# Optimization experiments

Measured on AMD Instinct MI355X. Metric: run time of the kernel, lower is better.

## Reference

```python
import jax, jax.numpy as jnp
import numpy as np

N = 100000
E = 500000
HID = 256
N_EDGE_TYPES = 5
N_ATOM = 16
N_CHARGE = 7
NUM_RBF = 16
CUTOFF = 5.0
LN_EPS = 1e-5


def _xavier(key, shape):
    fan_in, fan_out = shape[0], shape[1]
    lim = float(np.sqrt(6.0 / (fan_in + fan_out)))
    return jax.random.uniform(key, shape, jnp.float32, -lim, lim)


def setup_inputs() -> dict:
    key = jax.random.key(0)
    ks = jax.random.split(key, 12)
    input_dim = HID * 2 + NUM_RBF + N_ATOM + N_CHARGE  # 551
    h = jax.random.normal(ks[0], (N, HID), jnp.float32)
    x = jax.random.normal(ks[1], (N, 3), jnp.float32)
    spawn_node_idx = jax.random.randint(ks[2], (E,), 0, N)
    existing_node_idx = jax.random.randint(ks[3], (E,), 0, N)
    ins_x = jax.random.normal(ks[4], (E, 3), jnp.float32)
    ins_a = jax.random.randint(ks[5], (E,), 0, N_ATOM)
    ins_c = jax.random.randint(ks[6], (E,), 0, N_CHARGE)
    # MLP params (Xavier weights, zero biases; LayerNorm gamma=1, beta=0)
    W1 = _xavier(ks[7], (input_dim, HID)); b1 = jnp.zeros((HID,), jnp.float32)
    g1 = jnp.ones((HID,), jnp.float32); be1 = jnp.zeros((HID,), jnp.float32)
    W2 = _xavier(ks[8], (HID, HID // 2)); b2 = jnp.zeros((HID // 2,), jnp.float32)
    g2 = jnp.ones((HID // 2,), jnp.float32); be2 = jnp.zeros((HID // 2,), jnp.float32)
    W3 = _xavier(ks[9], (HID // 2, N_EDGE_TYPES)); b3 = jnp.zeros((N_EDGE_TYPES,), jnp.float32)
    # Gaussian RBF parameters: centers on [0, cutoff], shared width from spacing
    rbf_mu = jnp.linspace(0.0, CUTOFF, NUM_RBF).astype(jnp.float32)
    delta = CUTOFF / (NUM_RBF - 1)
    rbf_gamma = jnp.asarray(1.0 / (2.0 * delta * delta), jnp.float32)
    return {"h": h, "x": x, "spawn_node_idx": spawn_node_idx,
            "existing_node_idx": existing_node_idx, "ins_x": ins_x,
            "ins_a": ins_a, "ins_c": ins_c,
            "W1": W1, "b1": b1, "g1": g1, "be1": be1,
            "W2": W2, "b2": b2, "g2": g2, "be2": be2,
            "W3": W3, "b3": b3, "rbf_mu": rbf_mu, "rbf_gamma": rbf_gamma}


def _layer_norm(z, gamma, beta):
    mu = jnp.mean(z, axis=-1, keepdims=True)
    var = jnp.mean((z - mu) ** 2, axis=-1, keepdims=True)
    return (z - mu) * jax.lax.rsqrt(var + LN_EPS) * gamma + beta


def reference(h, x, spawn_node_idx, existing_node_idx, ins_x, ins_a, ins_c,
              W1, b1, g1, be1, W2, b2, g2, be2, W3, b3, rbf_mu, rbf_gamma):
    # gather node pairs  [E, HID] / [E, 3]
    h_spawn = h[spawn_node_idx]
    h_existing = h[existing_node_idx]
    existing_pos = x[existing_node_idx]
    # distance + Gaussian RBF  [E, NUM_RBF]
    d = jnp.maximum(jnp.linalg.norm(ins_x - existing_pos, axis=-1), 1e-6)
    dist_features = jnp.exp(-rbf_gamma * (d[:, None] - rbf_mu) ** 2)
    # one-hot insertion type features
    ins_atom = jax.nn.one_hot(ins_a, N_ATOM, dtype=h.dtype)
    ins_charge = jax.nn.one_hot(ins_c, N_CHARGE, dtype=h.dtype)
    feats = jnp.concatenate([h_spawn, h_existing, dist_features, ins_atom, ins_charge], axis=-1)
    # 3-layer MLP: Linear -> LN -> SiLU -> Linear -> LN -> SiLU -> Linear
    z = jax.nn.silu(_layer_norm(feats @ W1 + b1, g1, be1))
    z = jax.nn.silu(_layer_norm(z @ W2 + b2, g2, be2))
    return z @ W3 + b3  # [E, N_EDGE_TYPES]
```

## Files before the change

### kernel.cpp

```cpp
#include <hip/hip_runtime.h>
#include <stdint.h>

#define NN 100000
#define EE 500000
#define HIDD 256
#define LN_EPS 1e-5f

typedef _Float16 half8 __attribute__((ext_vector_type(8)));
typedef _Float16 half4 __attribute__((ext_vector_type(4)));
typedef __fp16 fp16x2 __attribute__((ext_vector_type(2)));
typedef float f32x4 __attribute__((ext_vector_type(4)));
typedef float f32x2 __attribute__((ext_vector_type(2)));

#define LBAR() asm volatile("s_waitcnt lgkmcnt(0)\n\ts_barrier" ::: "memory")

__device__ __forceinline__ unsigned short f2h(float f) {
  _Float16 h = (_Float16)f;
  union { _Float16 hh; unsigned short us; } u; u.hh = h;
  return u.us;
}

__device__ __forceinline__ unsigned pkrtz(float a, float b) {
  union { fp16x2 h; unsigned u; } c;
  c.h = __builtin_amdgcn_cvt_pkrtz(a, b);
  return c.u;
}

__device__ __forceinline__ float fast_silu(float y) {
  float e = __expf(-y);
  return y * __builtin_amdgcn_rcpf(1.f + e);
}

__device__ __forceinline__ half8 ldg8(const unsigned short* p) {
  return *(const half8*)p;
}

__device__ __forceinline__ int4 cvt_row(const float* s) {
  float4 a0 = *(const float4*)s, a1 = *(const float4*)(s + 4);
  uint4 ua;
  ua.x = pkrtz(a0.x, a0.y); ua.y = pkrtz(a0.z, a0.w);
  ua.z = pkrtz(a1.x, a1.y); ua.w = pkrtz(a1.z, a1.w);
  return *(int4*)&ua;
}

__global__ __launch_bounds__(256) void prep_kern(const float* __restrict__ h,
                                                 const float* __restrict__ W1,
                                                 const float* __restrict__ W2,
                                                 const float* __restrict__ W3,
                                                 unsigned short* __restrict__ hb,
                                                 unsigned short* __restrict__ w1sw,
                                                 unsigned short* __restrict__ w2sw,
                                                 unsigned short* __restrict__ w3sw) {
  int b = blockIdx.x;
  if (b < 712) {
    int t = b * 256 + threadIdx.x;
    if (t < 147456) {
      int chunk = t >> 14, rem = t & 16383;
      int kq = rem >> 11, n = (rem >> 3) & 255, j = rem & 7;
      int k = (chunk << 6) + (kq << 3) + j;
      float v = (k < 551) ? W1[k * 256 + n] : 0.f;
      w1sw[t] = f2h(v);
    } else if (t < 147456 + 32768) {
      int t2 = t - 147456;
      int chunk = t2 >> 13, rem = t2 & 8191;
      int kq = rem >> 10, n = (rem >> 3) & 127, j = rem & 7;
      int k = (chunk << 6) + (kq << 3) + j;
      w2sw[t2] = f2h(W2[k * 128 + n]);
    } else if (t < 147456 + 32768 + 2048) {
      int t3 = t - 180224;
      int kq = t3 >> 7, o = (t3 >> 3) & 15, j = t3 & 7;
      int k = (kq << 3) + j;
      w3sw[t3] = f2h((o < 5) ? W3[k * 5 + o] : 0.f);
    }
  } else {
    int i = ((b - 712) * 256 + threadIdx.x) * 8;
    float4 v0 = *(const float4*)(h + i);
    float4 v1 = *(const float4*)(h + i + 4);
    uint4 u;
    u.x = pkrtz(v0.x, v0.y); u.y = pkrtz(v0.z, v0.w);
    u.z = pkrtz(v1.x, v1.y); u.w = pkrtz(v1.z, v1.w);
    *(uint4*)(hb + i) = u;
  }
}

struct __align__(16) SMem {
  short r1[16384];
  short feats[4096];
  float red[512];
  _Float16 b1h[256], g1h[256], be1h[256];
  _Float16 b2h[128], g2h[128], be2h[128];
  float muv[16];
  float b3v[8];
  int spI[64], exI[64];
};

__global__ __launch_bounds__(256, 3)
void edge_head_main(const float* __restrict__ h, const float* __restrict__ x,
                    const int* __restrict__ spawn, const int* __restrict__ exist,
                    const float* __restrict__ insx, const int* __restrict__ insa,
                    const int* __restrict__ insc,
                    const float* __restrict__ b1, const float* __restrict__ g1,
                    const float* __restrict__ be1,
                    const float* __restrict__ b2, const float* __restrict__ g2,
                    const float* __restrict__ be2,
                    const float* __restrict__ b3, const float* __restrict__ mu,
                    const float* __restrict__ gammaP,
                    const unsigned short* __restrict__ w1sw,
                    const unsigned short* __restrict__ w2sw,
                    const unsigned short* __restrict__ w3swg,
                    const unsigned short* __restrict__ hb, int use_hb,
                    float* __restrict__ out) {
  __shared__ SMem sm;
  const int t = threadIdx.x;
  const int base = blockIdx.x * 64;
  const int lane = t & 63;
  const int wv = t >> 6;
  const int cl = lane & 15;
  const int q = lane >> 4;
  const int sx = (cl & 7) << 3;

  sm.b1h[t] = (_Float16)b1[t]; sm.g1h[t] = (_Float16)g1[t]; sm.be1h[t] = (_Float16)be1[t];
  if (t < 128) { sm.b2h[t] = (_Float16)b2[t]; sm.g2h[t] = (_Float16)g2[t]; sm.be2h[t] = (_Float16)be2[t]; }
  if (t < 16) sm.muv[t] = mu[t];
  if (t < 8) sm.b3v[t] = (t < 5) ? b3[t] : 0.f;
  if (t < 64) {
    int e = base + t; int ec = e < EE ? e : EE - 1;
    sm.spI[t] = spawn[ec]; sm.exI[t] = exist[ec];
  }
  const float gma = gammaP[0];

  LBAR();

  float dreg = 0.f;
  int k1 = 16, k2 = 32;
  if (t < 64) {
    int e = base + t; int ec = e < EE ? e : EE - 1;
    float ix0 = insx[ec * 3], ix1 = insx[ec * 3 + 1], ix2 = insx[ec * 3 + 2];
    int nd = sm.exI[t];
    float dx = ix0 - x[nd * 3], dy = ix1 - x[nd * 3 + 1], dz = ix2 - x[nd * 3 + 2];
    dreg = fmaxf(sqrtf(dx * dx + dy * dy + dz * dz), 1e-6f);
    k1 = 16 + insa[ec]; k2 = 32 + insc[ec];
  }

  const int row0 = t >> 3, p0 = t & 7;
  const int row1 = row0 + 32;
  const int sw0 = ((p0 ^ (row0 & 7)) << 3);
  const int sw1 = ((p0 ^ (row1 & 7)) << 3);

  const size_t oSp0 = (size_t)sm.spI[row0] * HIDD + p0 * 8;
  const size_t oSp1 = (size_t)sm.spI[row1] * HIDD + p0 * 8;
  const size_t oEx0 = (size_t)sm.exI[row0] * HIDD + p0 * 8;
  const size_t oEx1 = (size_t)sm.exI[row1] * HIDD + p0 * 8;
  const char* bSp0 = use_hb ? (const char*)(hb + oSp0) : (const char*)(h + oSp0);
  const char* bSp1 = use_hb ? (const char*)(hb + oSp1) : (const char*)(h + oSp1);
  const char* bEx0 = use_hb ? (const char*)(hb + oEx0) : (const char*)(h + oEx0);
  const char* bEx1 = use_hb ? (const char*)(hb + oEx1) : (const char*)(h + oEx1);

  int4 pS0, pS1, pS2, pS3;
#define GLOAD2(ph) do {                                                 \
    const char* b0_ = ((ph) < 2) ? bSp0 : bEx0;                         \
    const char* b1_ = ((ph) < 2) ? bSp1 : bEx1;                         \
    const int ce_ = ((ph) & 1) * 128;             \
    if (use_hb) {                                                       \
      pS0 = *(const int4*)(b0_ + ce_ * 2);                              \
      pS1 = *(const int4*)(b1_ + ce_ * 2);                              \
      pS2 = *(const int4*)(b0_ + (ce_ + 64) * 2);                       \
      pS3 = *(const int4*)(b1_ + (ce_ + 64) * 2);                       \
    } else {                                                            \
      pS0 = cvt_row((const float*)(b0_ + ce_ * 4));                     \
      pS1 = cvt_row((const float*)(b1_ + ce_ * 4));                     \
      pS2 = cvt_row((const float*)(b0_ + (ce_ + 64) * 4));              \
      pS3 = cvt_row((const float*)(b1_ + (ce_ + 64) * 4));              \
    }                                                                   \
  } while (0)

  GLOAD2(0);
  *(int4*)&sm.r1[row0 * 64 + sw0] = pS0;
  *(int4*)&sm.r1[row1 * 64 + sw1] = pS1;
  *(int4*)&sm.r1[4096 + row0 * 64 + sw0] = pS2;
  *(int4*)&sm.r1[4096 + row1 * 64 + sw1] = pS3;
  GLOAD2(1);

  const unsigned short* w1p = w1sw + q * 2048 + wv * 512 + cl * 8;

  if (t < 64) {
    short* rp = &sm.feats[t * 64];
    const int sw = t & 7;
    float rb[16];
#pragma unroll
    for (int k = 0; k < 16; ++k) { float dd = dreg - sm.muv[k]; rb[k] = __expf(-gma * dd * dd); }
    uint4 ua, ub;
    ua.x = pkrtz(rb[0], rb[1]);  ua.y = pkrtz(rb[2], rb[3]);
    ua.z = pkrtz(rb[4], rb[5]);  ua.w = pkrtz(rb[6], rb[7]);
    ub.x = pkrtz(rb[8], rb[9]);  ub.y = pkrtz(rb[10], rb[11]);
    ub.z = pkrtz(rb[12], rb[13]); ub.w = pkrtz(rb[14], rb[15]);
    *(int4*)&rp[(0 ^ sw) * 8] = *(int4*)&ua;
    *(int4*)&rp[(1 ^ sw) * 8] = *(int4*)&ub;
    const int4 z4 = {0, 0, 0, 0};
#pragma unroll
    for (int g = 2; g < 8; ++g) *(int4*)&rp[(g ^ sw) * 8] = z4;
    rp[((k1 >> 3) ^ sw) * 8 + (k1 & 7)] = (short)0x3C00;
    rp[((k2 >> 3) ^ sw) * 8 + (k2 & 7)] = (short)0x3C00;
  }

  LBAR();

  f32x4 acc[4][4];
#pragma unroll
  for (int i = 0; i < 4; ++i)
#pragma unroll
    for (int j = 0; j < 4; ++j) acc[i][j] = (f32x4){0.f, 0.f, 0.f, 0.f};

#pragma unroll
  for (int p = 0; p < 4; ++p) {
    if (p < 3) {
      const int nb = ((p + 1) & 1) * 8192;
      *(int4*)&sm.r1[nb + row0 * 64 + sw0] = pS0;
      *(int4*)&sm.r1[nb + row1 * 64 + sw1] = pS1;
      *(int4*)&sm.r1[nb + 4096 + row0 * 64 + sw0] = pS2;
      *(int4*)&sm.r1[nb + 4096 + row1 * 64 + sw1] = pS3;
      if (p < 2) GLOAD2(p + 2);
    }
    const int cb = (p & 1) * 8192;
#pragma unroll
    for (int ch = 0; ch < 2; ++ch) {
      const unsigned short* wp = w1p + (2 * p + ch) * 16384;
#pragma unroll
      for (int ks = 0; ks < 2; ++ks) {
        half8 bf[4], fX[4];
#pragma unroll
        for (int j = 0; j < 4; ++j)
          bf[j] = *(const half8*)&sm.r1[cb + ch * 4096 + (j * 16 + cl) * 64 + ((ks * 32 + q * 8) ^ sx)];
#pragma unroll
        for (int i = 0; i < 4; ++i) fX[i] = ldg8(wp + ks * 8192 + i * 128);
#pragma unroll
        for (int i = 0; i < 4; ++i)
#pragma unroll
          for (int j = 0; j < 4; ++j)
            acc[i][j] = __builtin_amdgcn_mfma_f32_16x16x32_f16(fX[i], bf[j], acc[i][j], 0, 0, 0);
      }
    }
    if (p < 3) LBAR();
  }
#undef GLOAD2

  {
    const unsigned short* wp = w1p + 8 * 16384;
#pragma unroll
    for (int ks = 0; ks < 2; ++ks) {
      half8 bf[4], fX[4];
#pragma unroll
      for (int j = 0; j < 4; ++j)
        bf[j] = *(const half8*)&sm.feats[(j * 16 + cl) * 64 + ((ks * 32 + q * 8) ^ sx)];
#pragma unroll
      for (int i = 0; i < 4; ++i) fX[i] = ldg8(wp + ks * 8192 + i * 128);
#pragma unroll
      for (int i = 0; i < 4; ++i)
#pragma unroll
        for (int j = 0; j < 4; ++j)
          acc[i][j] = __builtin_amdgcn_mfma_f32_16x16x32_f16(fX[i], bf[j], acc[i][j], 0, 0, 0);
    }
  }

  f32x2 bb1[4][2];
#pragma unroll
  for (int i = 0; i < 4; ++i) {
    half4 b4 = *(const half4*)&sm.b1h[wv * 64 + i * 16 + q * 4];
    bb1[i][0] = (f32x2){(float)b4[0], (float)b4[1]};
    bb1[i][1] = (f32x2){(float)b4[2], (float)b4[3]};
  }
  float S1arr[4], Q1arr[4];
#pragma unroll
  for (int j = 0; j < 4; ++j) {
    f32x2 S2 = (f32x2){0.f, 0.f}, Q2 = (f32x2){0.f, 0.f};
#pragma unroll
    for (int i = 0; i < 4; ++i) {
      f32x2 v0 = (f32x2){acc[i][j][0], acc[i][j][1]} + bb1[i][0];
      f32x2 v1 = (f32x2){acc[i][j][2], acc[i][j][3]} + bb1[i][1];
      acc[i][j][0] = v0[0]; acc[i][j][1] = v0[1];
      acc[i][j][2] = v1[0]; acc[i][j][3] = v1[1];
      S2 += v0 + v1;
      Q2 += v0 * v0;
      Q2 += v1 * v1;
    }
    float S = S2[0] + S2[1], Q = Q2[0] + Q2[1];
    S += __shfl_xor(S, 16); S += __shfl_xor(S, 32);
    Q += __shfl_xor(Q, 16); Q += __shfl_xor(Q, 32);
    S1arr[j] = S; Q1arr[j] = Q;
  }
  if (q == 0) {
#pragma unroll
    for (int j = 0; j < 4; ++j) {
      sm.red[wv * 64 + j * 16 + cl] = S1arr[j];
      sm.red[256 + wv * 64 + j * 16 + cl] = Q1arr[j];
    }
  }
  LBAR();
  f32x2 rs1[4], mr1[4];
#pragma unroll
  for (int j = 0; j < 4; ++j) {
    int m = j * 16 + cl;
    float S = sm.red[m] + sm.red[64 + m] + sm.red[128 + m] + sm.red[192 + m];
    float Q = sm.red[256 + m] + sm.red[320 + m] + sm.red[384 + m] + sm.red[448 + m];
    float mn = S * (1.f / 256.f);
    float rs = rsqrtf(Q * (1.f / 256.f) - mn * mn + LN_EPS);
    rs1[j] = (f32x2){rs, rs};
    mr1[j] = (f32x2){-mn * rs, -mn * rs};
  }
#pragma unroll
  for (int i = 0; i < 4; ++i) {
    half4 g4 = *(const half4*)&sm.g1h[wv * 64 + i * 16 + q * 4];
    half4 e4 = *(const half4*)&sm.be1h[wv * 64 + i * 16 + q * 4];
    f32x2 gg0 = (f32x2){(float)g4[0], (float)g4[1]}, gg1 = (f32x2){(float)g4[2], (float)g4[3]};
    f32x2 ee0 = (f32x2){(float)e4[0], (float)e4[1]}, ee1 = (f32x2){(float)e4[2], (float)e4[3]};
#pragma unroll
    for (int j = 0; j < 4; ++j) {
      f32x2 v0 = (f32x2){acc[i][j][0], acc[i][j][1]};
      f32x2 v1 = (f32x2){acc[i][j][2], acc[i][j][3]};
      f32x2 t0 = v0 * rs1[j] + mr1[j];
      f32x2 t1 = v1 * rs1[j] + mr1[j];
      f32x2 y0 = t0 * gg0 + ee0;
      f32x2 y1 = t1 * gg1 + ee1;
      float s0 = fast_silu(y0[0]), s1 = fast_silu(y0[1]);
      float s2 = fast_silu(y1[0]), s3 = fast_silu(y1[1]);
      uint2 w; w.x = pkrtz(s0, s1); w.y = pkrtz(s2, s3);
      int m = j * 16 + cl;
      int k0 = wv * 64 + i * 16 + q * 4;
      *(uint2*)&sm.r1[m * 256 + (k0 ^ ((m & 7) << 3))] = w;
    }
  }
  LBAR();

  half8 af3[4];
#pragma unroll
  for (int ks = 0; ks < 4; ++ks)
    af3[ks] = ldg8(w3swg + (ks * 4 + q) * 128 + cl * 8);

  const unsigned short* w2p = w2sw + q * 1024 + wv * 256 + cl * 8;
  f32x4 acc2[2][4];
#pragma unroll
  for (int i = 0; i < 2; ++i)
#pragma unroll
    for (int j = 0; j < 4; ++j) acc2[i][j] = (f32x4){0.f, 0.f, 0.f, 0.f};
#pragma unroll
  for (int c2 = 0; c2 < 4; ++c2) {
#pragma unroll
    for (int ks = 0; ks < 2; ++ks) {
      half8 a0 = ldg8(w2p + c2 * 8192 + ks * 4096);
      half8 a1 = ldg8(w2p + c2 * 8192 + ks * 4096 + 128);
      half8 bf[4];
#pragma unroll
      for (int j = 0; j < 4; ++j)
        bf[j] = *(const half8*)&sm.r1[(j * 16 + cl) * 256 + ((c2 * 64 + ks * 32 + q * 8) ^ sx)];
#pragma unroll
      for (int j = 0; j < 4; ++j) {
        acc2[0][j] = __builtin_amdgcn_mfma_f32_16x16x32_f16(a0, bf[j], acc2[0][j], 0, 0, 0);
        acc2[1][j] = __builtin_amdgcn_mfma_f32_16x16x32_f16(a1, bf[j], acc2[1][j], 0, 0, 0);
      }
    }
  }

  f32x2 bb2[2][2];
#pragma unroll
  for (int i = 0; i < 2; ++i) {
    half4 b4 = *(const half4*)&sm.b2h[wv * 32 + i * 16 + q * 4];
    bb2[i][0] = (f32x2){(float)b4[0], (float)b4[1]};
    bb2[i][1] = (f32x2){(float)b4[2], (float)b4[3]};
  }
  float S2arr[4], Q2arr[4];
#pragma unroll
  for (int j = 0; j < 4; ++j) {
    f32x2 S2 = (f32x2){0.f, 0.f}, Q2 = (f32x2){0.f, 0.f};
#pragma unroll
    for (int i = 0; i < 2; ++i) {
      f32x2 v0 = (f32x2){acc2[i][j][0], acc2[i][j][1]} + bb2[i][0];
      f32x2 v1 = (f32x2){acc2[i][j][2], acc2[i][j][3]} + bb2[i][1];
      acc2[i][j][0] = v0[0]; acc2[i][j][1] = v0[1];
      acc2[i][j][2] = v1[0]; acc2[i][j][3] = v1[1];
      S2 += v0 + v1;
      Q2 += v0 * v0;
      Q2 += v1 * v1;
    }
    float S = S2[0] + S2[1], Q = Q2[0] + Q2[1];
    S += __shfl_xor(S, 16); S += __shfl_xor(S, 32);
    Q += __shfl_xor(Q, 16); Q += __shfl_xor(Q, 32);
    S2arr[j] = S; Q2arr[j] = Q;
  }
  if (q == 0) {
#pragma unroll
    for (int j = 0; j < 4; ++j) {
      sm.red[wv * 64 + j * 16 + cl] = S2arr[j];
      sm.red[256 + wv * 64 + j * 16 + cl] = Q2arr[j];
    }
  }
  LBAR();
  f32x2 rs2[4], mr2[4];
#pragma unroll
  for (int j = 0; j < 4; ++j) {
    int m = j * 16 + cl;
    float S = sm.red[m] + sm.red[64 + m] + sm.red[128 + m] + sm.red[192 + m];
    float Q = sm.red[256 + m] + sm.red[320 + m] + sm.red[384 + m] + sm.red[448 + m];
    float mn = S * (1.f / 128.f);
    float rs = rsqrtf(Q * (1.f / 128.f) - mn * mn + LN_EPS);
    rs2[j] = (f32x2){rs, rs};
    mr2[j] = (f32x2){-mn * rs, -mn * rs};
  }
#pragma unroll
  for (int i = 0; i < 2; ++i) {
    half4 g4 = *(const half4*)&sm.g2h[wv * 32 + i * 16 + q * 4];
    half4 e4 = *(const half4*)&sm.be2h[wv * 32 + i * 16 + q * 4];
    f32x2 gg0 = (f32x2){(float)g4[0], (float)g4[1]}, gg1 = (f32x2){(float)g4[2], (float)g4[3]};
    f32x2 ee0 = (f32x2){(float)e4[0], (float)e4[1]}, ee1 = (f32x2){(float)e4[2], (float)e4[3]};
#pragma unroll
    for (int j = 0; j < 4; ++j) {
      f32x2 v0 = (f32x2){acc2[i][j][0], acc2[i][j][1]};
      f32x2 v1 = (f32x2){acc2[i][j][2], acc2[i][j][3]};
      f32x2 t0 = v0 * rs2[j] + mr2[j];
      f32x2 t1 = v1 * rs2[j] + mr2[j];
      f32x2 y0 = t0 * gg0 + ee0;
      f32x2 y1 = t1 * gg1 + ee1;
      float s0 = fast_silu(y0[0]), s1 = fast_silu(y0[1]);
      float s2 = fast_silu(y1[0]), s3 = fast_silu(y1[1]);
      uint2 w; w.x = pkrtz(s0, s1); w.y = pkrtz(s2, s3);
      int m = j * 16 + cl;
      int k0 = wv * 32 + i * 16 + q * 4;
      *(uint2*)&sm.r1[m * 128 + (k0 ^ ((m & 7) << 3))] = w;
    }
  }
  LBAR();

  f32x4 a3 = (f32x4){0.f, 0.f, 0.f, 0.f};
  const int m3 = wv * 16 + cl;
  const int sx3 = (m3 & 7) << 3;
#pragma unroll
  for (int ks = 0; ks < 4; ++ks) {
    half8 bfv = *(const half8*)&sm.r1[m3 * 128 + ((ks * 32 + q * 8) ^ sx3)];
    a3 = __builtin_amdgcn_mfma_f32_16x16x32_f16(af3[ks], bfv, a3, 0, 0, 0);
  }
#pragma unroll
  for (int r = 0; r < 4; ++r) {
    int o = q * 4 + r;
    if (o < 5) sm.red[m3 * 5 + o] = a3[r] + sm.b3v[o];
  }
  LBAR();
  if (t < 80) {
    size_t g = (size_t)base * 5 + (size_t)t * 4;
    if (g + 4 <= (size_t)EE * 5) {
      *(float4*)(out + g) = *(const float4*)&sm.red[t * 4];
    } else {
#pragma unroll
      for (int u = 0; u < 4; ++u)
        if (g + u < (size_t)EE * 5) out[g + u] = sm.red[t * 4 + u];
    }
  }
}

extern "C" void kernel_launch(void* const* d_in, const int* in_sizes, int n_in,
                              void* d_out, int out_size, void* d_ws, size_t ws_size,
                              hipStream_t stream) {
  const float* h    = (const float*)d_in[0];
  const float* x    = (const float*)d_in[1];
  const int* spawn  = (const int*)d_in[2];
  const int* exist  = (const int*)d_in[3];
  const float* insx = (const float*)d_in[4];
  const int* insa   = (const int*)d_in[5];
  const int* insc   = (const int*)d_in[6];
  const float* W1   = (const float*)d_in[7];
  const float* b1   = (const float*)d_in[8];
  const float* g1   = (const float*)d_in[9];
  const float* be1  = (const float*)d_in[10];
  const float* W2   = (const float*)d_in[11];
  const float* b2   = (const float*)d_in[12];
  const float* g2   = (const float*)d_in[13];
  const float* be2  = (const float*)d_in[14];
  const float* W3   = (const float*)d_in[15];
  const float* b3   = (const float*)d_in[16];
  const float* mu   = (const float*)d_in[17];
  const float* gma  = (const float*)d_in[18];

  unsigned short* w1sw = (unsigned short*)d_ws;
  unsigned short* w2sw = w1sw + 147456;
  unsigned short* w3sw = w2sw + 32768;
  unsigned short* hb   = w3sw + 2048;
  const size_t need_hb = 364544ull + (size_t)NN * HIDD * 2ull;
  int use_hb = (ws_size >= need_hb) ? 1 : 0;

  prep_kern<<<use_hb ? 13212 : 712, 256, 0, stream>>>(h, W1, W2, W3, hb, w1sw, w2sw, w3sw);
  edge_head_main<<<7813, 256, 0, stream>>>(h, x, spawn, exist, insx, insa, insc,
                                           b1, g1, be1, b2, g2, be2, b3, mu, gma,
                                           w1sw, w2sw, w3sw, hb, use_hb,
                                           (float*)d_out);
}
```

Baseline: 421.8 us.

## Switch layer-1 and layer-2 GEMMs to 32x32x16 MFMA tiles with matching weight layout

Replaces the 16x16x32 f16 MFMA tiling of the first two MLP layers with 32x32x16 MFMA instructions. The prep kernel's swizzled layouts for W1 and W2 change to match the new per-lane operand layout, and the LayerNorm reductions and epilogues are reindexed to the 32x32 accumulator layout. The cross-lane reduction drops to one shuffle step. The aim is fewer MFMA and LDS operand loads per FLOP and better operand reuse, at the cost of larger 16-wide accumulators that raise register pressure.

```diff
diff --git a/kernel.cpp b/kernel.cpp
--- a/kernel.cpp
+++ b/kernel.cpp
@@ -11,6 +11,7 @@
 typedef __fp16 fp16x2 __attribute__((ext_vector_type(2)));
 typedef float f32x4 __attribute__((ext_vector_type(4)));
 typedef float f32x2 __attribute__((ext_vector_type(2)));
+typedef float f32x16 __attribute__((ext_vector_type(16)));
 
 #define LBAR() asm volatile("s_waitcnt lgkmcnt(0)\n\ts_barrier" ::: "memory")
 
@@ -55,17 +56,22 @@
   if (b < 712) {
     int t = b * 256 + threadIdx.x;
     if (t < 147456) {
-      int chunk = t >> 14, rem = t & 16383;
-      int kq = rem >> 11, n = (rem >> 3) & 255, j = rem & 7;
-      int k = (chunk << 6) + (kq << 3) + j;
-      float v = (k < 551) ? W1[k * 256 + n] : 0.f;
-      w1sw[t] = f2h(v);
+      int kstep = t >> 12;
+      int rem = t & 4095;
+      int m = rem >> 4;
+      int hi = (rem >> 3) & 1;
+      int j = t & 7;
+      int k = kstep * 16 + hi * 8 + j;
+      w1sw[t] = f2h((k < 551) ? W1[k * 256 + m] : 0.f);
     } else if (t < 147456 + 32768) {
       int t2 = t - 147456;
-      int chunk = t2 >> 13, rem = t2 & 8191;
-      int kq = rem >> 10, n = (rem >> 3) & 127, j = rem & 7;
-      int k = (chunk << 6) + (kq << 3) + j;
-      w2sw[t2] = f2h(W2[k * 128 + n]);
+      int kstep = t2 >> 11;
+      int rem = t2 & 2047;
+      int m = rem >> 4;
+      int hi = (rem >> 3) & 1;
+      int j = t2 & 7;
+      int k = kstep * 16 + hi * 8 + j;
+      w2sw[t2] = f2h(W2[k * 128 + m]);
     } else if (t < 147456 + 32768 + 2048) {
       int t3 = t - 180224;
       int kq = t3 >> 7, o = (t3 >> 3) & 15, j = t3 & 7;
@@ -117,7 +123,9 @@
   const int wv = t >> 6;
   const int cl = lane & 15;
   const int q = lane >> 4;
-  const int sx = (cl & 7) << 3;
+  const int l31 = lane & 31;
+  const int hi = lane >> 5;
+  const int sxr = (l31 & 7) << 3;
 
   sm.b1h[t] = (_Float16)b1[t]; sm.g1h[t] = (_Float16)g1[t]; sm.be1h[t] = (_Float16)be1[t];
   if (t < 128) { sm.b2h[t] = (_Float16)b2[t]; sm.g2h[t] = (_Float16)g2[t]; sm.be2h[t] = (_Float16)be2[t]; }
@@ -160,7 +168,7 @@
 #define GLOAD2(ph) do {                                                 \
     const char* b0_ = ((ph) < 2) ? bSp0 : bEx0;                         \
     const char* b1_ = ((ph) < 2) ? bSp1 : bEx1;                         \
-    const int ce_ = ((ph) & 1) * 128;             \
+    const int ce_ = ((ph) & 1) * 128;                                   \
     if (use_hb) {                                                       \
       pS0 = *(const int4*)(b0_ + ce_ * 2);                              \
       pS1 = *(const int4*)(b1_ + ce_ * 2);                              \
@@ -181,7 +189,7 @@
   *(int4*)&sm.r1[4096 + row1 * 64 + sw1] = pS3;
   GLOAD2(1);
 
-  const unsigned short* w1p = w1sw + q * 2048 + wv * 512 + cl * 8;
+  const unsigned short* w1p = w1sw + (wv * 64 + l31) * 16 + hi * 8;
 
   if (t < 64) {
     short* rp = &sm.feats[t * 64];
@@ -205,11 +213,13 @@
 
   LBAR();
 
-  f32x4 acc[4][4];
-#pragma unroll
-  for (int i = 0; i < 4; ++i)
-#pragma unroll
-    for (int j = 0; j < 4; ++j) acc[i][j] = (f32x4){0.f, 0.f, 0.f, 0.f};
+  f32x16 acc[2][2];
+#pragma unroll
+  for (int mt = 0; mt < 2; ++mt)
+#pragma unroll
+    for (int nt = 0; nt < 2; ++nt)
+#pragma unroll
+      for (int r = 0; r < 16; ++r) acc[mt][nt][r] = 0.f;
 
 #pragma unroll
   for (int p = 0; p < 4; ++p) {
@@ -224,207 +234,200 @@
     const int cb = (p & 1) * 8192;
 #pragma unroll
     for (int ch = 0; ch < 2; ++ch) {
-      const unsigned short* wp = w1p + (2 * p + ch) * 16384;
-#pragma unroll
-      for (int ks = 0; ks < 2; ++ks) {
-        half8 bf[4], fX[4];
-#pragma unroll
-        for (int j = 0; j < 4; ++j)
-          bf[j] = *(const half8*)&sm.r1[cb + ch * 4096 + (j * 16 + cl) * 64 + ((ks * 32 + q * 8) ^ sx)];
-#pragma unroll
-        for (int i = 0; i < 4; ++i) fX[i] = ldg8(wp + ks * 8192 + i * 128);
-#pragma unroll
-        for (int i = 0; i < 4; ++i)
-#pragma unroll
-          for (int j = 0; j < 4; ++j)
-            acc[i][j] = __builtin_amdgcn_mfma_f32_16x16x32_f16(fX[i], bf[j], acc[i][j], 0, 0, 0);
+      const int kc = 2 * p + ch;
+#pragma unroll
+      for (int sc = 0; sc < 4; ++sc) {
+        const int koff = sc * 16 + hi * 8;
+        half8 bf0 = *(const half8*)&sm.r1[cb + ch * 4096 + l31 * 64 + (koff ^ sxr)];
+        half8 bf1 = *(const half8*)&sm.r1[cb + ch * 4096 + (32 + l31) * 64 + (koff ^ sxr)];
+        half8 fX0 = ldg8(w1p + (kc * 4 + sc) * 4096);
+        half8 fX1 = ldg8(w1p + (kc * 4 + sc) * 4096 + 512);
+        acc[0][0] = __builtin_amdgcn_mfma_f32_32x32x16_f16(fX0, bf0, acc[0][0], 0, 0, 0);
+        acc[0][1] = __builtin_amdgcn_mfma_f32_32x32x16_f16(fX0, bf1, acc[0][1], 0, 0, 0);
+        acc[1][0] = __builtin_amdgcn_mfma_f32_32x32x16_f16(fX1, bf0, acc[1][0], 0, 0, 0);
+        acc[1][1] = __builtin_amdgcn_mfma_f32_32x32x16_f16(fX1, bf1, acc[1][1], 0, 0, 0);
       }
     }
     if (p < 3) LBAR();
   }
 #undef GLOAD2
 
+#pragma unroll
+  for (int sc = 0; sc < 4; ++sc) {
+    const int koff = sc * 16 + hi * 8;
+    half8 bf0 = *(const half8*)&sm.feats[l31 * 64 + (koff ^ sxr)];
+    half8 bf1 = *(const half8*)&sm.feats[(32 + l31) * 64 + (koff ^ sxr)];
+    half8 fX0 = ldg8(w1p + (32 + sc) * 4096);
+    half8 fX1 = ldg8(w1p + (32 + sc) * 4096 + 512);
+    acc[0][0] = __builtin_amdgcn_mfma_f32_32x32x16_f16(fX0, bf0, acc[0][0], 0, 0, 0);
+    acc[0][1] = __builtin_amdgcn_mfma_f32_32x32x16_f16(fX0, bf1, acc[0][1], 0, 0, 0);
+    acc[1][0] = __builtin_amdgcn_mfma_f32_32x32x16_f16(fX1, bf0, acc[1][0], 0, 0, 0);
+    acc[1][1] = __builtin_amdgcn_mfma_f32_32x32x16_f16(fX1, bf1, acc[1][1], 0, 0, 0);
+  }
+
+  float S1[2], Q1[2];
   {
-    const unsigned short* wp = w1p + 8 * 16384;
-#pragma unroll
-    for (int ks = 0; ks < 2; ++ks) {
-      half8 bf[4], fX[4];
-#pragma unroll
-      for (int j = 0; j < 4; ++j)
-        bf[j] = *(const half8*)&sm.feats[(j * 16 + cl) * 64 + ((ks * 32 + q * 8) ^ sx)];
-#pragma unroll
-      for (int i = 0; i < 4; ++i) fX[i] = ldg8(wp + ks * 8192 + i * 128);
-#pragma unroll
-      for (int i = 0; i < 4; ++i)
-#pragma unroll
-        for (int j = 0; j < 4; ++j)
-          acc[i][j] = __builtin_amdgcn_mfma_f32_16x16x32_f16(fX[i], bf[j], acc[i][j], 0, 0, 0);
-    }
-  }
-
-  f32x2 bb1[4][2];
-#pragma unroll
-  for (int i = 0; i < 4; ++i) {
-    half4 b4 = *(const half4*)&sm.b1h[wv * 64 + i * 16 + q * 4];
-    bb1[i][0] = (f32x2){(float)b4[0], (float)b4[1]};
-    bb1[i][1] = (f32x2){(float)b4[2], (float)b4[3]};
-  }
-  float S1arr[4], Q1arr[4];
-#pragma unroll
-  for (int j = 0; j < 4; ++j) {
-    f32x2 S2 = (f32x2){0.f, 0.f}, Q2 = (f32x2){0.f, 0.f};
-#pragma unroll
-    for (int i = 0; i < 4; ++i) {
-      f32x2 v0 = (f32x2){acc[i][j][0], acc[i][j][1]} + bb1[i][0];
-      f32x2 v1 = (f32x2){acc[i][j][2], acc[i][j][3]} + bb1[i][1];
-      acc[i][j][0] = v0[0]; acc[i][j][1] = v0[1];
-      acc[i][j][2] = v1[0]; acc[i][j][3] = v1[1];
-      S2 += v0 + v1;
-      Q2 += v0 * v0;
-      Q2 += v1 * v1;
-    }
-    float S = S2[0] + S2[1], Q = Q2[0] + Q2[1];
-    S += __shfl_xor(S, 16); S += __shfl_xor(S, 32);
-    Q += __shfl_xor(Q, 16); Q += __shfl_xor(Q, 32);
-    S1arr[j] = S; Q1arr[j] = Q;
-  }
-  if (q == 0) {
-#pragma unroll
-    for (int j = 0; j < 4; ++j) {
-      sm.red[wv * 64 + j * 16 + cl] = S1arr[j];
-      sm.red[256 + wv * 64 + j * 16 + cl] = Q1arr[j];
-    }
-  }
-  LBAR();
-  f32x2 rs1[4], mr1[4];
-#pragma unroll
-  for (int j = 0; j < 4; ++j) {
-    int m = j * 16 + cl;
-    float S = sm.red[m] + sm.red[64 + m] + sm.red[128 + m] + sm.red[192 + m];
-    float Q = sm.red[256 + m] + sm.red[320 + m] + sm.red[384 + m] + sm.red[448 + m];
+    f32x2 s2[2] = {{0.f, 0.f}, {0.f, 0.f}};
+    f32x2 q2[2] = {{0.f, 0.f}, {0.f, 0.f}};
+#pragma unroll
+    for (int mt = 0; mt < 2; ++mt)
+#pragma unroll
+      for (int g = 0; g < 4; ++g) {
+        half4 b4 = *(const half4*)&sm.b1h[wv * 64 + mt * 32 + 8 * g + 4 * hi];
+        f32x2 bb0 = (f32x2){(float)b4[0], (float)b4[1]};
+        f32x2 bb1 = (f32x2){(float)b4[2], (float)b4[3]};
+#pragma unroll
+        for (int nt = 0; nt < 2; ++nt) {
+          f32x2 v0 = (f32x2){acc[mt][nt][4 * g + 0], acc[mt][nt][4 * g + 1]} + bb0;
+          f32x2 v1 = (f32x2){acc[mt][nt][4 * g + 2], acc[mt][nt][4 * g + 3]} + bb1;
+          acc[mt][nt][4 * g + 0] = v0[0]; acc[mt][nt][4 * g + 1] = v0[1];
+          acc[mt][nt][4 * g + 2] = v1[0]; acc[mt][nt][4 * g + 3] = v1[1];
+          s2[nt] += v0 + v1;
+          q2[nt] += v0 * v0;
+          q2[nt] += v1 * v1;
+        }
+      }
+#pragma unroll
+    for (int nt = 0; nt < 2; ++nt) {
+      float S = s2[nt][0] + s2[nt][1], Q = q2[nt][0] + q2[nt][1];
+      S += __shfl_xor(S, 32);
+      Q += __shfl_xor(Q, 32);
+      S1[nt] = S; Q1[nt] = Q;
+    }
+  }
+  if (hi == 0) {
+#pragma unroll
+    for (int nt = 0; nt < 2; ++nt) {
+      sm.red[wv * 64 + nt * 32 + l31] = S1[nt];
+      sm.red[256 + wv * 64 + nt * 32 + l31] = Q1[nt];
+    }
+  }
+  LBAR();
+  f32x2 rs1[2], mr1[2];
+#pragma unroll
+  for (int nt = 0; nt < 2; ++nt) {
+    int e = nt * 32 + l31;
+    float S = sm.red[e] + sm.red[64 + e] + sm.red[128 + e] + sm.red[192 + e];
+    float Q = sm.red[256 + e] + sm.red[320 + e] + sm.red[384 + e] + sm.red[448 + e];
     float mn = S * (1.f / 256.f);
     float rs = rsqrtf(Q * (1.f / 256.f) - mn * mn + LN_EPS);
-    rs1[j] = (f32x2){rs, rs};
-    mr1[j] = (f32x2){-mn * rs, -mn * rs};
-  }
-#pragma unroll
-  for (int i = 0; i < 4; ++i) {
-    half4 g4 = *(const half4*)&sm.g1h[wv * 64 + i * 16 + q * 4];
-    half4 e4 = *(const half4*)&sm.be1h[wv * 64 + i * 16 + q * 4];
+    rs1[nt] = (f32x2){rs, rs};
+    mr1[nt] = (f32x2){-mn * rs, -mn * rs};
+  }
+#pragma unroll
+  for (int mt = 0; mt < 2; ++mt)
+#pragma unroll
+    for (int g = 0; g < 4; ++g) {
+      const int cb4 = wv * 64 + mt * 32 + 8 * g + 4 * hi;
+      half4 g4 = *(const half4*)&sm.g1h[cb4];
+      half4 e4 = *(const half4*)&sm.be1h[cb4];
+      f32x2 gg0 = (f32x2){(float)g4[0], (float)g4[1]}, gg1 = (f32x2){(float)g4[2], (float)g4[3]};
+      f32x2 ee0 = (f32x2){(float)e4[0], (float)e4[1]}, ee1 = (f32x2){(float)e4[2], (float)e4[3]};
+#pragma unroll
+      for (int nt = 0; nt < 2; ++nt) {
+        f32x2 v0 = (f32x2){acc[mt][nt][4 * g + 0], acc[mt][nt][4 * g + 1]};
+        f32x2 v1 = (f32x2){acc[mt][nt][4 * g + 2], acc[mt][nt][4 * g + 3]};
+        f32x2 t0 = v0 * rs1[nt] + mr1[nt];
+        f32x2 t1 = v1 * rs1[nt] + mr1[nt];
+        f32x2 y0 = t0 * gg0 + ee0;
+        f32x2 y1 = t1 * gg1 + ee1;
+        float s0 = fast_silu(y0[0]), s1 = fast_silu(y0[1]);
+        float s2v = fast_silu(y1[0]), s3 = fast_silu(y1[1]);
+        uint2 w; w.x = pkrtz(s0, s1); w.y = pkrtz(s2v, s3);
+        int m = nt * 32 + l31;
+        *(uint2*)&sm.r1[m * 256 + (cb4 ^ ((m & 7) << 3))] = w;
+      }
+    }
+  LBAR();
+
+  half8 af3[4];
+#pragma unroll
+  for (int ks = 0; ks < 4; ++ks)
+    af3[ks] = ldg8(w3swg + (ks * 4 + q) * 128 + cl * 8);
+
+  const unsigned short* w2p = w2sw + (wv * 32 + l31) * 16 + hi * 8;
+  f32x16 acc2[2];
+#pragma unroll
+  for (int nt = 0; nt < 2; ++nt)
+#pragma unroll
+    for (int r = 0; r < 16; ++r) acc2[nt][r] = 0.f;
+#pragma unroll
+  for (int ks = 0; ks < 16; ++ks) {
+    const int koff = ks * 16 + hi * 8;
+    half8 a0 = ldg8(w2p + ks * 2048);
+    half8 bf0 = *(const half8*)&sm.r1[l31 * 256 + (koff ^ sxr)];
+    half8 bf1 = *(const half8*)&sm.r1[(32 + l31) * 256 + (koff ^ sxr)];
+    acc2[0] = __builtin_amdgcn_mfma_f32_32x32x16_f16(a0, bf0, acc2[0], 0, 0, 0);
+    acc2[1] = __builtin_amdgcn_mfma_f32_32x32x16_f16(a0, bf1, acc2[1], 0, 0, 0);
+  }
+
+  float S2a[2], Q2a[2];
+  {
+    f32x2 s2[2] = {{0.f, 0.f}, {0.f, 0.f}};
+    f32x2 q2[2] = {{0.f, 0.f}, {0.f, 0.f}};
+#pragma unroll
+    for (int g = 0; g < 4; ++g) {
+      half4 b4 = *(const half4*)&sm.b2h[wv * 32 + 8 * g + 4 * hi];
+      f32x2 bb0 = (f32x2){(float)b4[0], (float)b4[1]};
+      f32x2 bb1 = (f32x2){(float)b4[2], (float)b4[3]};
+#pragma unroll
+      for (int nt = 0; nt < 2; ++nt) {
+        f32x2 v0 = (f32x2){acc2[nt][4 * g + 0], acc2[nt][4 * g + 1]} + bb0;
+        f32x2 v1 = (f32x2){acc2[nt][4 * g + 2], acc2[nt][4 * g + 3]} + bb1;
+        acc2[nt][4 * g + 0] = v0[0]; acc2[nt][4 * g + 1] = v0[1];
+        acc2[nt][4 * g + 2] = v1[0]; acc2[nt][4 * g + 3] = v1[1];
+        s2[nt] += v0 + v1;
+        q2[nt] += v0 * v0;
+        q2[nt] += v1 * v1;
+      }
+    }
+#pragma unroll
+    for (int nt = 0; nt < 2; ++nt) {
+      float S = s2[nt][0] + s2[nt][1], Q = q2[nt][0] + q2[nt][1];
+      S += __shfl_xor(S, 32);
+      Q += __shfl_xor(Q, 32);
+      S2a[nt] = S; Q2a[nt] = Q;
+    }
+  }
+  if (hi == 0) {
+#pragma unroll
+    for (int nt = 0; nt < 2; ++nt) {
+      sm.red[wv * 64 + nt * 32 + l31] = S2a[nt];
+      sm.red[256 + wv * 64 + nt * 32 + l31] = Q2a[nt];
+    }
+  }
+  LBAR();
+  f32x2 rs2[2], mr2[2];
+#pragma unroll
+  for (int nt = 0; nt < 2; ++nt) {
+    int e = nt * 32 + l31;
+    float S = sm.red[e] + sm.red[64 + e] + sm.red[128 + e] + sm.red[192 + e];
+    float Q = sm.red[256 + e] + sm.red[320 + e] + sm.red[384 + e] + sm.red[448 + e];
+    float mn = S * (1.f / 128.f);
+    float rs = rsqrtf(Q * (1.f / 128.f) - mn * mn + LN_EPS);
+    rs2[nt] = (f32x2){rs, rs};
+    mr2[nt] = (f32x2){-mn * rs, -mn * rs};
+  }
+#pragma unroll
+  for (int g = 0; g < 4; ++g) {
+    const int cb4 = wv * 32 + 8 * g + 4 * hi;
+    half4 g4 = *(const half4*)&sm.g2h[cb4];
+    half4 e4 = *(const half4*)&sm.be2h[cb4];
     f32x2 gg0 = (f32x2){(float)g4[0], (float)g4[1]}, gg1 = (f32x2){(float)g4[2], (float)g4[3]};
     f32x2 ee0 = (f32x2){(float)e4[0], (float)e4[1]}, ee1 = (f32x2){(float)e4[2], (float)e4[3]};
 #pragma unroll
-    for (int j = 0; j < 4; ++j) {
-      f32x2 v0 = (f32x2){acc[i][j][0], acc[i][j][1]};
-      f32x2 v1 = (f32x2){acc[i][j][2], acc[i][j][3]};
-      f32x2 t0 = v0 * rs1[j] + mr1[j];
-      f32x2 t1 = v1 * rs1[j] + mr1[j];
+    for (int nt = 0; nt < 2; ++nt) {
+      f32x2 v0 = (f32x2){acc2[nt][4 * g + 0], acc2[nt][4 * g + 1]};
+      f32x2 v1 = (f32x2){acc2[nt][4 * g + 2], acc2[nt][4 * g + 3]};
+      f32x2 t0 = v0 * rs2[nt] + mr2[nt];
+      f32x2 t1 = v1 * rs2[nt] + mr2[nt];
       f32x2 y0 = t0 * gg0 + ee0;
       f32x2 y1 = t1 * gg1 + ee1;
       float s0 = fast_silu(y0[0]), s1 = fast_silu(y0[1]);
-      float s2 = fast_silu(y1[0]), s3 = fast_silu(y1[1]);
-      uint2 w; w.x = pkrtz(s0, s1); w.y = pkrtz(s2, s3);
-      int m = j * 16 + cl;
-      int k0 = wv * 64 + i * 16 + q * 4;
-      *(uint2*)&sm.r1[m * 256 + (k0 ^ ((m & 7) << 3))] = w;
-    }
-  }
-  LBAR();
-
-  half8 af3[4];
-#pragma unroll
-  for (int ks = 0; ks < 4; ++ks)
-    af3[ks] = ldg8(w3swg + (ks * 4 + q) * 128 + cl * 8);
-
-  const unsigned short* w2p = w2sw + q * 1024 + wv * 256 + cl * 8;
-  f32x4 acc2[2][4];
-#pragma unroll
-  for (int i = 0; i < 2; ++i)
-#pragma unroll
-    for (int j = 0; j < 4; ++j) acc2[i][j] = (f32x4){0.f, 0.f, 0.f, 0.f};
-#pragma unroll
-  for (int c2 = 0; c2 < 4; ++c2) {
-#pragma unroll
-    for (int ks = 0; ks < 2; ++ks) {
-      half8 a0 = ldg8(w2p + c2 * 8192 + ks * 4096);
-      half8 a1 = ldg8(w2p + c2 * 8192 + ks * 4096 + 128);
-      half8 bf[4];
-#pragma unroll
-      for (int j = 0; j < 4; ++j)
-        bf[j] = *(const half8*)&sm.r1[(j * 16 + cl) * 256 + ((c2 * 64 + ks * 32 + q * 8) ^ sx)];
-#pragma unroll
-      for (int j = 0; j < 4; ++j) {
-        acc2[0][j] = __builtin_amdgcn_mfma_f32_16x16x32_f16(a0, bf[j], acc2[0][j], 0, 0, 0);
-        acc2[1][j] = __builtin_amdgcn_mfma_f32_16x16x32_f16(a1, bf[j], acc2[1][j], 0, 0, 0);
-      }
-    }
-  }
-
-  f32x2 bb2[2][2];
-#pragma unroll
-  for (int i = 0; i < 2; ++i) {
-    half4 b4 = *(const half4*)&sm.b2h[wv * 32 + i * 16 + q * 4];
-    bb2[i][0] = (f32x2){(float)b4[0], (float)b4[1]};
-    bb2[i][1] = (f32x2){(float)b4[2], (float)b4[3]};
-  }
-  float S2arr[4], Q2arr[4];
-#pragma unroll
-  for (int j = 0; j < 4; ++j) {
-    f32x2 S2 = (f32x2){0.f, 0.f}, Q2 = (f32x2){0.f, 0.f};
-#pragma unroll
-    for (int i = 0; i < 2; ++i) {
-      f32x2 v0 = (f32x2){acc2[i][j][0], acc2[i][j][1]} + bb2[i][0];
-      f32x2 v1 = (f32x2){acc2[i][j][2], acc2[i][j][3]} + bb2[i][1];
-      acc2[i][j][0] = v0[0]; acc2[i][j][1] = v0[1];
-      acc2[i][j][2] = v1[0]; acc2[i][j][3] = v1[1];
-      S2 += v0 + v1;
-      Q2 += v0 * v0;
-      Q2 += v1 * v1;
-    }
-    float S = S2[0] + S2[1], Q = Q2[0] + Q2[1];
-    S += __shfl_xor(S, 16); S += __shfl_xor(S, 32);
-    Q += __shfl_xor(Q, 16); Q += __shfl_xor(Q, 32);
-    S2arr[j] = S; Q2arr[j] = Q;
-  }
-  if (q == 0) {
-#pragma unroll
-    for (int j = 0; j < 4; ++j) {
-      sm.red[wv * 64 + j * 16 + cl] = S2arr[j];
-      sm.red[256 + wv * 64 + j * 16 + cl] = Q2arr[j];
-    }
-  }
-  LBAR();
-  f32x2 rs2[4], mr2[4];
-#pragma unroll
-  for (int j = 0; j < 4; ++j) {
-    int m = j * 16 + cl;
-    float S = sm.red[m] + sm.red[64 + m] + sm.red[128 + m] + sm.red[192 + m];
-    float Q = sm.red[256 + m] + sm.red[320 + m] + sm.red[384 + m] + sm.red[448 + m];
-    float mn = S * (1.f / 128.f);
-    float rs = rsqrtf(Q * (1.f / 128.f) - mn * mn + LN_EPS);
-    rs2[j] = (f32x2){rs, rs};
-    mr2[j] = (f32x2){-mn * rs, -mn * rs};
-  }
-#pragma unroll
-  for (int i = 0; i < 2; ++i) {
-    half4 g4 = *(const half4*)&sm.g2h[wv * 32 + i * 16 + q * 4];
-    half4 e4 = *(const half4*)&sm.be2h[wv * 32 + i * 16 + q * 4];
-    f32x2 gg0 = (f32x2){(float)g4[0], (float)g4[1]}, gg1 = (f32x2){(float)g4[2], (float)g4[3]};
-    f32x2 ee0 = (f32x2){(float)e4[0], (float)e4[1]}, ee1 = (f32x2){(float)e4[2], (float)e4[3]};
-#pragma unroll
-    for (int j = 0; j < 4; ++j) {
-      f32x2 v0 = (f32x2){acc2[i][j][0], acc2[i][j][1]};
-      f32x2 v1 = (f32x2){acc2[i][j][2], acc2[i][j][3]};
-      f32x2 t0 = v0 * rs2[j] + mr2[j];
-      f32x2 t1 = v1 * rs2[j] + mr2[j];
-      f32x2 y0 = t0 * gg0 + ee0;
-      f32x2 y1 = t1 * gg1 + ee1;
-      float s0 = fast_silu(y0[0]), s1 = fast_silu(y0[1]);
-      float s2 = fast_silu(y1[0]), s3 = fast_silu(y1[1]);
-      uint2 w; w.x = pkrtz(s0, s1); w.y = pkrtz(s2, s3);
-      int m = j * 16 + cl;
-      int k0 = wv * 32 + i * 16 + q * 4;
-      *(uint2*)&sm.r1[m * 128 + (k0 ^ ((m & 7) << 3))] = w;
+      float s2v = fast_silu(y1[0]), s3 = fast_silu(y1[1]);
+      uint2 w; w.x = pkrtz(s0, s1); w.y = pkrtz(s2v, s3);
+      int m = nt * 32 + l31;
+      *(uint2*)&sm.r1[m * 128 + (cb4 ^ ((m & 7) << 3))] = w;
     }
   }
   LBAR();
```

After: 451.1 us. 1.07x slower.
